# Kernel tuning notes

Measured on AMD Instinct MI355X. Metric: run time of the kernel, lower is better.

## Reference

```python
import jax, jax.numpy as jnp
import numpy as np

N_FFT = 4096
HOP = 1024
HALF = N_FFT // 2  # 2048; also number of freq bins is HALF+1 = 2049


def _make_kernels():
    # Periodic hann window, matching torch.hann_window(N) default (periodic=True)
    n = np.arange(N_FFT, dtype=np.float32)
    window = 0.5 * (1.0 - np.cos(2.0 * np.pi * n / N_FFT))
    freqs = np.arange(HALF + 1, dtype=np.float32)[:, None]  # [K,1]
    omega = 2.0 * np.pi * freqs * n[None, :] / N_FFT        # [K, n_fft]
    scale = np.float32(1.0 / np.sqrt(N_FFT))                # normalized=True
    cos_k = (np.cos(omega) * window[None, :] * scale).astype(np.float32)
    sin_k = (-np.sin(omega) * window[None, :] * scale).astype(np.float32)
    return jnp.asarray(cos_k), jnp.asarray(sin_k)


def setup_inputs() -> dict:
    key = jax.random.key(0)
    x = jax.random.normal(key, (32, 1, 441000), dtype=jnp.float32)
    cos_kernel, sin_kernel = _make_kernels()  # each [2049, 4096]
    return {"x": x, "cos_kernel": cos_kernel, "sin_kernel": sin_kernel}


def reference(x, cos_kernel, sin_kernel):
    # center=True: reflect-pad half_n_fft on each side of the time axis
    xp = jnp.pad(x, ((0, 0), (0, 0), (HALF, HALF)), mode='reflect')  # [B,1,L]
    L = xp.shape[-1]
    num_frames = (L - N_FFT) // HOP + 1
    # Frame extraction (equivalent to stride-HOP conv1d with width-N_FFT kernels)
    idx = HOP * jnp.arange(num_frames)[:, None] + jnp.arange(N_FFT)[None, :]  # [F, n_fft]
    frames = xp[:, 0, :][:, idx]  # [B, F, n_fft]
    real = jnp.einsum('bfn,kn->bkf', frames, cos_kernel)  # [B, 2049, F]
    imag = jnp.einsum('bfn,kn->bkf', frames, sin_kernel)  # [B, 2049, F]
    return jnp.stack((real, imag), axis=-1)  # [B, 2049, F, 2]
```

## Files before the change

### kernel.cpp

```cpp
#include <hip/hip_runtime.h>
#include <math.h>

#define NFFT  4096
#define MHALF 2048
#define HOPSZ 1024
#define LX    441000
#define NB    32
#define NF    431
#define NK    2049
#define NFPB  8
#define FBLK  54
#define NWG3  (NB * FBLK)
#define CH3   (NWG3 / 8)

#define SW(A) ((A) ^ (((A) >> 4) & 0xF))
#define WAVESYNC() do { asm volatile("s_waitcnt lgkmcnt(0)" ::: "memory"); \
                        __builtin_amdgcn_sched_barrier(0); } while (0)

typedef __fp16 half2v __attribute__((ext_vector_type(2)));

__device__ __forceinline__ float2 cadd(float2 a, float2 b){ return make_float2(a.x+b.x, a.y+b.y); }
__device__ __forceinline__ float2 csub(float2 a, float2 b){ return make_float2(a.x-b.x, a.y-b.y); }
__device__ __forceinline__ float2 cmul(float2 a, float2 b){
  return make_float2(fmaf(a.x, b.x, -(a.y*b.y)), fmaf(a.x, b.y, a.y*b.x));
}
#define STH(ptr, idx, v) (ptr)[idx] = __builtin_amdgcn_cvt_pkrtz((v).x, (v).y)
__device__ __forceinline__ float2 ldh(const half2v* __restrict__ X, int idx) {
  half2v h = X[idx];
  return make_float2((float)h.x, (float)h.y);
}

constexpr float W32C[22] = {
  1.0f, 0.98078528040323f, 0.92387953251129f, 0.83146961230255f, 0.70710678118655f,
  0.55557023301960f, 0.38268343236509f, 0.19509032201613f, 0.0f, -0.19509032201613f,
  -0.38268343236509f, -0.55557023301960f, -0.70710678118655f, -0.83146961230255f,
  -0.92387953251129f, -0.98078528040323f, -1.0f, -0.98078528040323f,
  -0.92387953251129f, -0.83146961230255f, -0.70710678118655f, -0.55557023301960f };
constexpr float W32S[22] = {
  0.0f, 0.19509032201613f, 0.38268343236509f, 0.55557023301960f, 0.70710678118655f,
  0.83146961230255f, 0.92387953251129f, 0.98078528040323f, 1.0f, 0.98078528040323f,
  0.92387953251129f, 0.83146961230255f, 0.70710678118655f, 0.55557023301960f,
  0.38268343236509f, 0.19509032201613f, 0.0f, -0.19509032201613f,
  -0.38268343236509f, -0.55557023301960f, -0.70710678118655f, -0.83146961230255f };

template<int N> __device__ __forceinline__ float2 w32m(float2 z) {
  if constexpr (N == 0) { return z; }
  else if constexpr (N == 8) { return make_float2(z.y, -z.x); }
  else {
    constexpr float c = W32C[N];
    constexpr float s = W32S[N];
    return make_float2(fmaf(z.x, c, z.y * s), fmaf(z.y, c, -(z.x * s)));
  }
}

__global__ void stft_init(float* __restrict__ ws) {
  int i = blockIdx.x * blockDim.x + threadIdx.x;
  const double PI = 3.14159265358979323846;
  if (i < 4096) {
    double w = 0.5 * (1.0 - cos(2.0 * PI * (double)i / 4096.0)) * (1.0 / 64.0);
    ws[i] = (float)w;
  }
  if (i < 1024) {
    double a = -2.0 * PI * (double)i / 2048.0;
    ws[4096 + 2 * i]     = (float)cos(a);
    ws[4096 + 2 * i + 1] = (float)sin(a);
  }
  if (i < 2049) {
    double a = -2.0 * PI * (double)i / 4096.0;
    ws[6144 + 2 * i]     = (float)cos(a);
    ws[6144 + 2 * i + 1] = (float)sin(a);
  }
}

__device__ __forceinline__ void dft8(const float2* a, float2* B) {
  float2 t0 = cadd(a[0], a[4]), t1 = csub(a[0], a[4]);
  float2 t2 = cadd(a[2], a[6]), t3 = csub(a[2], a[6]);
  float2 t4 = cadd(a[1], a[5]), t5 = csub(a[1], a[5]);
  float2 t6 = cadd(a[3], a[7]), t7 = csub(a[3], a[7]);
  const float K = 0.70710678118654752f;
  float2 wt5  = make_float2(K * (t5.x + t5.y), K * (t5.y - t5.x));
  float2 w3t7 = make_float2(K * (t7.y - t7.x), -K * (t7.x + t7.y));
  float2 wt7  = make_float2(K * (t7.x + t7.y), K * (t7.y - t7.x));
  float2 w3t5 = make_float2(K * (t5.y - t5.x), -K * (t5.x + t5.y));
  float2 e0 = cadd(t0, t2), e1 = csub(t0, t2);
  float2 f0 = cadd(t4, t6), f1 = csub(t4, t6);
  B[0] = cadd(e0, f0);
  B[4] = csub(e0, f0);
  B[2] = make_float2(e1.x + f1.y, e1.y - f1.x);
  B[6] = make_float2(e1.x - f1.y, e1.y + f1.x);
  float2 g0 = make_float2(t1.x + t3.y, t1.y - t3.x);
  float2 g1 = make_float2(t1.x - t3.y, t1.y + t3.x);
  float2 h0 = cadd(wt5, w3t7);
  float2 h1 = cadd(wt7, w3t5);
  B[1] = cadd(g0, h0);
  B[5] = csub(g0, h0);
  B[3] = cadd(g1, h1);
  B[7] = csub(g1, h1);
}

template<int S>
__device__ __forceinline__ void bf8(half2v* __restrict__ X, int sxor,
                                    const float2* __restrict__ twg,
                                    int j, const float2* a) {
  const int q = j & (S - 1);
  const int t = j - q;
  float2 B[8];
  dft8(a, B);
  float2 w1 = twg[t];
  float2 w2 = cmul(w1, w1);
  float2 w3 = cmul(w2, w1);
  float2 w4 = cmul(w2, w2);
  float2 w5 = cmul(w3, w2);
  float2 w6 = cmul(w3, w3);
  float2 w7 = cmul(w4, w3);
  const int o = q + 8 * t;
  STH(X, SW(o) ^ sxor, B[0]);
  { float2 v = cmul(w1, B[1]); STH(X, SW(o + S)     ^ sxor, v); }
  { float2 v = cmul(w2, B[2]); STH(X, SW(o + 2 * S) ^ sxor, v); }
  { float2 v = cmul(w3, B[3]); STH(X, SW(o + 3 * S) ^ sxor, v); }
  { float2 v = cmul(w4, B[4]); STH(X, SW(o + 4 * S) ^ sxor, v); }
  { float2 v = cmul(w5, B[5]); STH(X, SW(o + 5 * S) ^ sxor, v); }
  { float2 v = cmul(w6, B[6]); STH(X, SW(o + 6 * S) ^ sxor, v); }
  { float2 v = cmul(w7, B[7]); STH(X, SW(o + 7 * S) ^ sxor, v); }
}

#define VBLK(V) do {                                                  \
    float2 tt[8], BB[8];                                              \
    tt[0] = d[8*(V)+0];                                               \
    tt[1] = w32m<1*(V)>(d[8*(V)+1]);                                  \
    tt[2] = w32m<2*(V)>(d[8*(V)+2]);                                  \
    tt[3] = w32m<3*(V)>(d[8*(V)+3]);                                  \
    tt[4] = w32m<4*(V)>(d[8*(V)+4]);                                  \
    tt[5] = w32m<5*(V)>(d[8*(V)+5]);                                  \
    tt[6] = w32m<6*(V)>(d[8*(V)+6]);                                  \
    tt[7] = w32m<7*(V)>(d[8*(V)+7]);                                  \
    dft8(tt, BB);                                                     \
    STH(sl, SW(l + (((V) +  0) << 6)) ^ sxor, BB[0]);                 \
    STH(sl, SW(l + (((V) +  4) << 6)) ^ sxor, BB[1]);                 \
    STH(sl, SW(l + (((V) +  8) << 6)) ^ sxor, BB[2]);                 \
    STH(sl, SW(l + (((V) + 12) << 6)) ^ sxor, BB[3]);                 \
    STH(sl, SW(l + (((V) + 16) << 6)) ^ sxor, BB[4]);                 \
    STH(sl, SW(l + (((V) + 20) << 6)) ^ sxor, BB[5]);                 \
    STH(sl, SW(l + (((V) + 24) << 6)) ^ sxor, BB[6]);                 \
    STH(sl, SW(l + (((V) + 28) << 6)) ^ sxor, BB[7]);                 \
  } while (0)

__global__ __launch_bounds__(512) void stft_fft(const float* __restrict__ x,
                                                const float* __restrict__ ws,
                                                float* __restrict__ out) {
  __shared__ half2v fbuf[NFPB * 2048];

  const int tid = threadIdx.x;
  const int wid = (blockIdx.x & 7) * CH3 + (blockIdx.x >> 3);
  const int b  = wid / FBLK;
  const int fb = wid - b * FBLK;
  const int f0 = fb * NFPB;
  const int wv = tid >> 6;
  const int l  = tid & 63;
  const int f  = f0 + wv;

  const float*  win  = ws;
  const float2* winv = (const float2*)ws;
  const float2* twg  = (const float2*)(ws + 4096);
  const float2* tw4  = (const float2*)(ws + 6144);
  const float* xb = x + (size_t)b * LX;

  if (f < NF) {
    half2v* __restrict__ sl = &fbuf[wv * 2048];
    const int sxor = wv << 2;
    const int base = f * HOPSZ - MHALF;

    float2 a[4][8];
    if (base >= 0 && base + NFFT <= LX) {
      const float2* xv = (const float2*)(xb + base);
#pragma unroll
      for (int r = 0; r < 4; ++r) {
        const int j = l + (r << 6);
#pragma unroll
        for (int m = 0; m < 8; ++m) {
          const int idx = j + (m << 8);
          float2 v = xv[idx];
          float2 w = winv[idx];
          a[r][m] = make_float2(v.x * w.x, v.y * w.y);
        }
      }
    } else {
#pragma unroll
      for (int r = 0; r < 4; ++r) {
        const int j = l + (r << 6);
#pragma unroll
        for (int m = 0; m < 8; ++m) {
          const int idx = j + (m << 8);
          int s0 = base + 2 * idx;
          int s1 = s0 + 1;
          s0 = (s0 < 0) ? -s0 : ((s0 >= LX) ? (2 * LX - 2 - s0) : s0);
          s1 = (s1 < 0) ? -s1 : ((s1 >= LX) ? (2 * LX - 2 - s1) : s1);
          a[r][m] = make_float2(xb[s0] * win[2 * idx], xb[s1] * win[2 * idx + 1]);
        }
      }
    }
#pragma unroll
    for (int r = 0; r < 4; ++r) bf8<1>(sl, sxor, twg, l + (r << 6), a[r]);
    WAVESYNC();

#pragma unroll
    for (int r = 0; r < 4; ++r) {
      const int j = l + (r << 6);
#pragma unroll
      for (int m = 0; m < 8; ++m) a[r][m] = ldh(sl, SW(j + (m << 8)) ^ sxor);
    }
    WAVESYNC();
#pragma unroll
    for (int r = 0; r < 4; ++r) bf8<8>(sl, sxor, twg, l + (r << 6), a[r]);
    WAVESYNC();

    float2 d[32];
#pragma unroll
    for (int m = 0; m < 32; ++m) d[m] = ldh(sl, SW(l + (m << 6)) ^ sxor);
#pragma unroll
    for (int m1 = 0; m1 < 8; ++m1) {
      float2 p0 = d[m1], p1 = d[m1 + 8], p2 = d[m1 + 16], p3 = d[m1 + 24];
      float2 e0 = cadd(p0, p2), e1 = csub(p0, p2);
      float2 o0 = cadd(p1, p3), o1 = csub(p1, p3);
      d[m1]      = cadd(e0, o0);
      d[m1 + 8]  = make_float2(e1.x + o1.y, e1.y - o1.x);
      d[m1 + 16] = csub(e0, o0);
      d[m1 + 24] = make_float2(e1.x - o1.y, e1.y + o1.x);
    }
    VBLK(0); VBLK(1); VBLK(2); VBLK(3);
  }
  __syncthreads();

  float2* __restrict__ op = (float2*)out;
  const size_t obB = (size_t)b * NK * NF;
  const int s  = tid & 7;
  const int kk = tid >> 3;
  const int fS = f0 + s;
  const bool act = (fS < NF);
  const half2v* __restrict__ sl2 = &fbuf[s * 2048];
  const int sx2 = s << 2;
#pragma unroll 4
  for (int it = 0; it < 16; ++it) {
    const int k  = kk + (it << 6);
    const int km = (2048 - k) & 2047;
    float2 zk = ldh(sl2, SW(k)  ^ sx2);
    float2 zm = ldh(sl2, SW(km) ^ sx2);
    float xex = 0.5f * (zk.x + zm.x);
    float xey = 0.5f * (zk.y - zm.y);
    float xox = 0.5f * (zk.y + zm.y);
    float xoy = 0.5f * (zm.x - zk.x);
    float2 w = tw4[k];
    float tx = w.x * xox - w.y * xoy;
    float ty = w.x * xoy + w.y * xox;
    if (act) {
      op[obB + (size_t)k * NF + fS]          = make_float2(xex + tx,  xey + ty);
      op[obB + (size_t)(2048 - k) * NF + fS] = make_float2(xex - tx, -xey + ty);
    }
  }
  if (tid < 8 && (f0 + tid) < NF) {
    const half2v* slt = &fbuf[tid * 2048];
    float2 zq = ldh(slt, SW(1024) ^ (tid << 2));
    op[obB + (size_t)1024 * NF + (f0 + tid)] = make_float2(zq.x, -zq.y);
  }
}

extern "C" void kernel_launch(void* const* d_in, const int* in_sizes, int n_in,
                              void* d_out, int out_size, void* d_ws, size_t ws_size,
                              hipStream_t stream) {
  const float* x = (const float*)d_in[0];
  float* ws = (float*)d_ws;
  float* out = (float*)d_out;
  stft_init<<<16, 256, 0, stream>>>(ws);
  stft_fft<<<NWG3, 512, 0, stream>>>(x, ws, out);
}
```

Before: 137.3 us.

## Process two STFT frames per wave with 256-thread workgroups

Each wave now computes the FFT of two frames, interleaving their loads, butterflies and LDS traffic, and the workgroup shrinks to 256 threads while still covering eight frames. The output write-back loop is doubled to cover the same bins with half the threads. The intent is more instruction-level parallelism per wave and less per-frame overhead. It costs higher register pressure, a risk of spilling, and fewer waves to hide latency.

Result: faster. 129.2 us (-5.9%).

```diff
diff --git a/kernel.cpp b/kernel.cpp
--- a/kernel.cpp
+++ b/kernel.cpp
@@ -124,30 +124,78 @@
   { float2 v = cmul(w7, B[7]); STH(X, SW(o + 7 * S) ^ sxor, v); }
 }
 
-#define VBLK(V) do {                                                  \
+__device__ __forceinline__ void loadwin(float2 (*a)[8], const float* __restrict__ xb,
+                                        int f, int l,
+                                        const float2* __restrict__ winv,
+                                        const float* __restrict__ win) {
+  const int base = f * HOPSZ - MHALF;
+  if (base >= 0 && base + NFFT <= LX) {
+    const float2* xv = (const float2*)(xb + base);
+#pragma unroll
+    for (int r = 0; r < 4; ++r) {
+      const int j = l + (r << 6);
+#pragma unroll
+      for (int m = 0; m < 8; ++m) {
+        const int idx = j + (m << 8);
+        float2 v = xv[idx];
+        float2 w = winv[idx];
+        a[r][m] = make_float2(v.x * w.x, v.y * w.y);
+      }
+    }
+  } else {
+#pragma unroll
+    for (int r = 0; r < 4; ++r) {
+      const int j = l + (r << 6);
+#pragma unroll
+      for (int m = 0; m < 8; ++m) {
+        const int idx = j + (m << 8);
+        int s0 = base + 2 * idx;
+        int s1 = s0 + 1;
+        s0 = (s0 < 0) ? -s0 : ((s0 >= LX) ? (2 * LX - 2 - s0) : s0);
+        s1 = (s1 < 0) ? -s1 : ((s1 >= LX) ? (2 * LX - 2 - s1) : s1);
+        a[r][m] = make_float2(xb[s0] * win[2 * idx], xb[s1] * win[2 * idx + 1]);
+      }
+    }
+  }
+}
+
+#define VBLK(dd, slp, sx, V) do {                                     \
     float2 tt[8], BB[8];                                              \
-    tt[0] = d[8*(V)+0];                                               \
-    tt[1] = w32m<1*(V)>(d[8*(V)+1]);                                  \
-    tt[2] = w32m<2*(V)>(d[8*(V)+2]);                                  \
-    tt[3] = w32m<3*(V)>(d[8*(V)+3]);                                  \
-    tt[4] = w32m<4*(V)>(d[8*(V)+4]);                                  \
-    tt[5] = w32m<5*(V)>(d[8*(V)+5]);                                  \
-    tt[6] = w32m<6*(V)>(d[8*(V)+6]);                                  \
-    tt[7] = w32m<7*(V)>(d[8*(V)+7]);                                  \
+    tt[0] = dd[8*(V)+0];                                              \
+    tt[1] = w32m<1*(V)>(dd[8*(V)+1]);                                 \
+    tt[2] = w32m<2*(V)>(dd[8*(V)+2]);                                 \
+    tt[3] = w32m<3*(V)>(dd[8*(V)+3]);                                 \
+    tt[4] = w32m<4*(V)>(dd[8*(V)+4]);                                 \
+    tt[5] = w32m<5*(V)>(dd[8*(V)+5]);                                 \
+    tt[6] = w32m<6*(V)>(dd[8*(V)+6]);                                 \
+    tt[7] = w32m<7*(V)>(dd[8*(V)+7]);                                 \
     dft8(tt, BB);                                                     \
-    STH(sl, SW(l + (((V) +  0) << 6)) ^ sxor, BB[0]);                 \
-    STH(sl, SW(l + (((V) +  4) << 6)) ^ sxor, BB[1]);                 \
-    STH(sl, SW(l + (((V) +  8) << 6)) ^ sxor, BB[2]);                 \
-    STH(sl, SW(l + (((V) + 12) << 6)) ^ sxor, BB[3]);                 \
-    STH(sl, SW(l + (((V) + 16) << 6)) ^ sxor, BB[4]);                 \
-    STH(sl, SW(l + (((V) + 20) << 6)) ^ sxor, BB[5]);                 \
-    STH(sl, SW(l + (((V) + 24) << 6)) ^ sxor, BB[6]);                 \
-    STH(sl, SW(l + (((V) + 28) << 6)) ^ sxor, BB[7]);                 \
+    STH(slp, SW(l + (((V) +  0) << 6)) ^ sx, BB[0]);                  \
+    STH(slp, SW(l + (((V) +  4) << 6)) ^ sx, BB[1]);                  \
+    STH(slp, SW(l + (((V) +  8) << 6)) ^ sx, BB[2]);                  \
+    STH(slp, SW(l + (((V) + 12) << 6)) ^ sx, BB[3]);                  \
+    STH(slp, SW(l + (((V) + 16) << 6)) ^ sx, BB[4]);                  \
+    STH(slp, SW(l + (((V) + 20) << 6)) ^ sx, BB[5]);                  \
+    STH(slp, SW(l + (((V) + 24) << 6)) ^ sx, BB[6]);                  \
+    STH(slp, SW(l + (((V) + 28) << 6)) ^ sx, BB[7]);                  \
   } while (0)
 
-__global__ __launch_bounds__(512) void stft_fft(const float* __restrict__ x,
-                                                const float* __restrict__ ws,
-                                                float* __restrict__ out) {
+#define DFT4PASS(dd) do {                                             \
+    _Pragma("unroll")                                                 \
+    for (int m1 = 0; m1 < 8; ++m1) {                                  \
+      float2 p0 = dd[m1], p1 = dd[m1 + 8], p2 = dd[m1 + 16], p3 = dd[m1 + 24]; \
+      float2 e0 = cadd(p0, p2), e1 = csub(p0, p2);                    \
+      float2 o0 = cadd(p1, p3), o1 = csub(p1, p3);                    \
+      dd[m1]      = cadd(e0, o0);                                     \
+      dd[m1 + 8]  = make_float2(e1.x + o1.y, e1.y - o1.x);            \
+      dd[m1 + 16] = csub(e0, o0);                                     \
+      dd[m1 + 24] = make_float2(e1.x - o1.y, e1.y + o1.x);            \
+    }                                                                 \
+  } while (0)
+
+__global__ __launch_bounds__(256, 2) void stft_fft(const float* __restrict__ x,
+                                                   const float* __restrict__ ws,
+                                                   float* __restrict__ out) {
   __shared__ half2v fbuf[NFPB * 2048];
 
   const int tid = threadIdx.x;
@@ -157,7 +205,9 @@
   const int f0 = fb * NFPB;
   const int wv = tid >> 6;
   const int l  = tid & 63;
-  const int f  = f0 + wv;
+  const int fA = f0 + 2 * wv;
+  const int fB = fA + 1;
+  const bool hasB = (fB < NF);
 
   const float*  win  = ws;
   const float2* winv = (const float2*)ws;
@@ -165,69 +215,56 @@
   const float2* tw4  = (const float2*)(ws + 6144);
   const float* xb = x + (size_t)b * LX;
 
-  if (f < NF) {
-    half2v* __restrict__ sl = &fbuf[wv * 2048];
-    const int sxor = wv << 2;
-    const int base = f * HOPSZ - MHALF;
-
-    float2 a[4][8];
-    if (base >= 0 && base + NFFT <= LX) {
-      const float2* xv = (const float2*)(xb + base);
-#pragma unroll
-      for (int r = 0; r < 4; ++r) {
-        const int j = l + (r << 6);
-#pragma unroll
-        for (int m = 0; m < 8; ++m) {
-          const int idx = j + (m << 8);
-          float2 v = xv[idx];
-          float2 w = winv[idx];
-          a[r][m] = make_float2(v.x * w.x, v.y * w.y);
-        }
+  half2v* __restrict__ slA = &fbuf[(2 * wv) * 2048];
+  half2v* __restrict__ slB = &fbuf[(2 * wv + 1) * 2048];
+  const int sxA = (2 * wv) << 2;
+  const int sxB = (2 * wv + 1) << 2;
+
+  {
+    float2 aA[4][8], aB[4][8];
+    loadwin(aA, xb, fA, l, winv, win);
+    if (hasB) loadwin(aB, xb, fB, l, winv, win);
+#pragma unroll
+    for (int r = 0; r < 4; ++r) {
+      bf8<1>(slA, sxA, twg, l + (r << 6), aA[r]);
+      if (hasB) bf8<1>(slB, sxB, twg, l + (r << 6), aB[r]);
+    }
+    WAVESYNC();
+
+#pragma unroll
+    for (int r = 0; r < 4; ++r) {
+      const int j = l + (r << 6);
+#pragma unroll
+      for (int m = 0; m < 8; ++m) {
+        aA[r][m] = ldh(slA, SW(j + (m << 8)) ^ sxA);
+        if (hasB) aB[r][m] = ldh(slB, SW(j + (m << 8)) ^ sxB);
       }
-    } else {
-#pragma unroll
-      for (int r = 0; r < 4; ++r) {
-        const int j = l + (r << 6);
-#pragma unroll
-        for (int m = 0; m < 8; ++m) {
-          const int idx = j + (m << 8);
-          int s0 = base + 2 * idx;
-          int s1 = s0 + 1;
-          s0 = (s0 < 0) ? -s0 : ((s0 >= LX) ? (2 * LX - 2 - s0) : s0);
-          s1 = (s1 < 0) ? -s1 : ((s1 >= LX) ? (2 * LX - 2 - s1) : s1);
-          a[r][m] = make_float2(xb[s0] * win[2 * idx], xb[s1] * win[2 * idx + 1]);
-        }
-      }
-    }
-#pragma unroll
-    for (int r = 0; r < 4; ++r) bf8<1>(sl, sxor, twg, l + (r << 6), a[r]);
+    }
     WAVESYNC();
-
-#pragma unroll
-    for (int r = 0; r < 4; ++r) {
-      const int j = l + (r << 6);
-#pragma unroll
-      for (int m = 0; m < 8; ++m) a[r][m] = ldh(sl, SW(j + (m << 8)) ^ sxor);
+#pragma unroll
+    for (int r = 0; r < 4; ++r) {
+      bf8<8>(slA, sxA, twg, l + (r << 6), aA[r]);
+      if (hasB) bf8<8>(slB, sxB, twg, l + (r << 6), aB[r]);
     }
     WAVESYNC();
-#pragma unroll
-    for (int r = 0; r < 4; ++r) bf8<8>(sl, sxor, twg, l + (r << 6), a[r]);
+  }
+
+  {
+    float2 dA[32], dB[32];
+#pragma unroll
+    for (int m = 0; m < 32; ++m) {
+      dA[m] = ldh(slA, SW(l + (m << 6)) ^ sxA);
+      if (hasB) dB[m] = ldh(slB, SW(l + (m << 6)) ^ sxB);
+    }
     WAVESYNC();
-
-    float2 d[32];
-#pragma unroll
-    for (int m = 0; m < 32; ++m) d[m] = ldh(sl, SW(l + (m << 6)) ^ sxor);
-#pragma unroll
-    for (int m1 = 0; m1 < 8; ++m1) {
-      float2 p0 = d[m1], p1 = d[m1 + 8], p2 = d[m1 + 16], p3 = d[m1 + 24];
-      float2 e0 = cadd(p0, p2), e1 = csub(p0, p2);
-      float2 o0 = cadd(p1, p3), o1 = csub(p1, p3);
-      d[m1]      = cadd(e0, o0);
-      d[m1 + 8]  = make_float2(e1.x + o1.y, e1.y - o1.x);
-      d[m1 + 16] = csub(e0, o0);
-      d[m1 + 24] = make_float2(e1.x - o1.y, e1.y + o1.x);
-    }
-    VBLK(0); VBLK(1); VBLK(2); VBLK(3);
+    DFT4PASS(dA);
+    VBLK(dA, slA, sxA, 0); VBLK(dA, slA, sxA, 1);
+    VBLK(dA, slA, sxA, 2); VBLK(dA, slA, sxA, 3);
+    if (hasB) {
+      DFT4PASS(dB);
+      VBLK(dB, slB, sxB, 0); VBLK(dB, slB, sxB, 1);
+      VBLK(dB, slB, sxB, 2); VBLK(dB, slB, sxB, 3);
+    }
   }
   __syncthreads();
 
@@ -240,8 +277,8 @@
   const half2v* __restrict__ sl2 = &fbuf[s * 2048];
   const int sx2 = s << 2;
 #pragma unroll 4
-  for (int it = 0; it < 16; ++it) {
-    const int k  = kk + (it << 6);
+  for (int it = 0; it < 32; ++it) {
+    const int k  = kk + (it << 5);
     const int km = (2048 - k) & 2047;
     float2 zk = ldh(sl2, SW(k)  ^ sx2);
     float2 zm = ldh(sl2, SW(km) ^ sx2);
@@ -271,5 +308,5 @@
   float* ws = (float*)d_ws;
   float* out = (float*)d_out;
   stft_init<<<16, 256, 0, stream>>>(ws);
-  stft_fft<<<NWG3, 512, 0, stream>>>(x, ws, out);
-}
+  stft_fft<<<NWG3, 256, 0, stream>>>(x, ws, out);
+}
```
